# Kernel tuning notes

Measured on AMD Instinct MI355X. Metric: run time of the kernel, lower is better.

## Reference

```python
import jax, jax.numpy as jnp
from jax import lax
import numpy as np

SHAPE = (64, 64, 64)  # spatial grid (D, H, W)
N_PTS = 100000        # active voxels
KPAD = (1, 2, 2)      # 'same' padding for (3,5,5) kernel


def _conv(x, w, pad):
    # x: [B,D,H,W,C], w: [kd,kh,kw,Cin,Cout]
    return lax.conv_general_dilated(
        x, w, window_strides=(1, 1, 1),
        padding=[(p, p) for p in pad],
        dimension_numbers=('NDHWC', 'DHWIO', 'NDHWC'))


def _sparse_maxpool2(x, mask):
    # spconv SparseMaxPool3d(2,2): output active where any input in 2x2x2
    # window is active; value = max over active inputs only.
    neg = jnp.float32(-1e30)
    xm = jnp.where(mask > 0, x, neg)
    win = (1, 2, 2, 2, 1)
    y = lax.reduce_window(xm, neg, lax.max, win, win, 'VALID')
    m2 = lax.reduce_window(mask, jnp.float32(0), lax.max, win, win, 'VALID')
    return jnp.where(m2 > 0, y, 0.0), m2


def setup_inputs() -> dict:
    rng = np.random.default_rng(0)
    D, H, W = SHAPE
    lin = rng.choice(D * H * W, size=N_PTS, replace=False)  # unique voxels
    z = lin // (H * W)
    y = (lin // W) % H
    x = lin % W
    coors = np.stack([np.zeros(N_PTS, np.int32), z, y, x], 1).astype(np.int32)

    key = jax.random.key(0)
    ks = jax.random.split(key, 16)
    feats = jax.random.normal(ks[0], (N_PTS, 3), jnp.float32)

    dims = [(3, 64), (64, 64), (64, 96), (96, 96), (96, 128), (128, 128),
            (128, 160), (160, 160), (160, 192), (192, 192), (192, 224),
            (224, 224), (224, 256), (256, 256)]
    inp = {'features': feats, 'coors': jnp.asarray(coors), 'batch_size': 1}
    for i, (ci, co) in enumerate(dims):
        scale = 1.0 / np.sqrt(ci * 75.0)  # 75 = 3*5*5 kernel taps
        inp[f'w{i}'] = jax.random.normal(ks[i + 1], (3, 5, 5, ci, co),
                                         jnp.float32) * scale
    return inp


def reference(features, coors, batch_size,
              w0, w1, w2, w3, w4, w5, w6, w7, w8, w9, w10, w11, w12, w13):
    # Densify the sparse tensor: inactive voxels are exactly zero, so a dense
    # conv followed by masking to the active set reproduces submanifold conv.
    b, z, y, x = coors[:, 0], coors[:, 1], coors[:, 2], coors[:, 3]
    dense = jnp.zeros((1,) + SHAPE + (3,), jnp.float32).at[b, z, y, x].set(features)
    mask = jnp.zeros((1,) + SHAPE + (1,), jnp.float32).at[b, z, y, x].set(1.0)

    ws = [w0, w1, w2, w3, w4, w5, w6, w7, w8, w9, w10, w11]
    h = dense
    wi = 0
    for _lvl in range(6):  # 6 (subm, subm, pool2) stages
        h = _conv(h, ws[wi], KPAD) * mask; wi += 1
        h = _conv(h, ws[wi], KPAD) * mask; wi += 1
        h, mask = _sparse_maxpool2(h, mask)

    # SparseConv3d(224,256,(3,5,5),padding=(1,2,2)): output active set is the
    # dilation of the input active set by the kernel footprint.
    m2 = lax.reduce_window(mask, jnp.float32(0), lax.max,
                           (1, 3, 5, 5, 1), (1, 1, 1, 1, 1),
                           [(0, 0), (1, 1), (2, 2), (2, 2), (0, 0)])
    h = _conv(h, w12, KPAD) * m2
    mask = m2
    # final SubMConv3d(256,256)
    h = _conv(h, w13, KPAD) * mask
    return h  # [1,1,1,1,256]
```

## Files before the change

kernel.cpp:

```cpp
#include <hip/hip_runtime.h>
#include <hip/hip_bf16.h>
#include <cstdint>

typedef __attribute__((ext_vector_type(8))) short bf16x8;
typedef __attribute__((ext_vector_type(4))) float f32x4;

__device__ __forceinline__ unsigned short f2bf_hi(float v) {
    unsigned u = __float_as_uint(v);
    u = u + 0x7fffu + ((u >> 16) & 1u);
    return (unsigned short)(u >> 16);
}
__device__ __forceinline__ float bf2f(unsigned short h) {
    return __uint_as_float(((unsigned)h) << 16);
}

__global__ void scatter_kernel(const float* __restrict__ feats,
                               const int* __restrict__ coors,
                               float* __restrict__ dense,
                               float* __restrict__ mask, int n)
{
    int i = blockIdx.x * blockDim.x + threadIdx.x;
    if (i >= n) return;
    const int z = coors[i * 4 + 1];
    const int y = coors[i * 4 + 2];
    const int x = coors[i * 4 + 3];
    const size_t s = (size_t)((z * 64 + y) * 64 + x);
    dense[s * 3 + 0] = feats[i * 3 + 0];
    dense[s * 3 + 1] = feats[i * 3 + 1];
    dense[s * 3 + 2] = feats[i * 3 + 2];
    mask[s] = 1.f;
}

__global__ void wprep_kernel(const float* __restrict__ w,
                             unsigned short* __restrict__ wv, int CI, int CO)
{
    const int total = 75 * CI * CO;
    const int stride = gridDim.x * blockDim.x;
    for (int i = blockIdx.x * blockDim.x + threadIdx.x; i < total; i += stride) {
        const int tap = i / (CI * CO);
        const int r = i - tap * CI * CO;
        const int ci = r / CO;
        const int co = r - ci * CO;
        const size_t o = ((size_t)(tap * (CI / 8) + (ci >> 3)) * CO + co) * 8 + (ci & 7);
        wv[o] = f2bf_hi(w[i]);
    }
}

__global__ void wprep2_kernel(const float* __restrict__ w,
                              unsigned short* __restrict__ wv, int CI, int CO)
{
    const int total = 75 * CI * CO;
    const int stride = gridDim.x * blockDim.x;
    for (int i = blockIdx.x * blockDim.x + threadIdx.x; i < total; i += stride) {
        const int tap = i / (CI * CO);
        const int r = i - tap * CI * CO;
        const int ci = r / CO;
        const int co = r - ci * CO;
        const float v = w[i];
        const unsigned short h = f2bf_hi(v);
        const unsigned short l = f2bf_hi(v - bf2f(h));
        const size_t o = ((size_t)(tap * (CI / 8) + (ci >> 3)) * CO + co) * 16 + (ci & 7);
        wv[o] = h; wv[o + 8] = l;
    }
}

__global__ __launch_bounds__(256)
void conv1_kernel(const float* __restrict__ in, const float* __restrict__ w,
                  const float* __restrict__ mask, unsigned short* __restrict__ ob)
{
    constexpr int S = 64, SP = 68;
    __shared__ float lds[15][3][SP];

    const int bid = blockIdx.y * S + blockIdx.x;
    const int wg = (bid & 7) * (S * S / 8) + (bid >> 3);
    const int y = wg & 63, z = wg >> 6;
    const int t = threadIdx.x;

    for (int idx = t; idx < 15 * 3 * SP; idx += 256) {
        const int r = idx / (3 * SP);
        const int rem = idx - r * 3 * SP;
        const int ci = rem / SP;
        const int x = rem - ci * SP;
        const int kz = r / 5, ky = r - kz * 5;
        const int zz = z + kz - 1, yy = y + ky - 2, xi = x - 2;
        float v = 0.f;
        if ((unsigned)zz < (unsigned)S && (unsigned)yy < (unsigned)S && (unsigned)xi < (unsigned)S)
            v = in[(size_t)((zz * S + yy) * S + xi) * 3 + ci];
        lds[r][ci][x] = v;
    }
    __syncthreads();

    const int co = t & 63, xs = t >> 6;
    float acc[16];
#pragma unroll
    for (int i = 0; i < 16; ++i) acc[i] = 0.f;

#pragma unroll 1
    for (int r = 0; r < 15; ++r) {
#pragma unroll
        for (int ci = 0; ci < 3; ++ci) {
            float inv[20];
#pragma unroll
            for (int j = 0; j < 5; ++j)
                *(float4*)&inv[j * 4] = *(const float4*)&lds[r][ci][xs * 16 + j * 4];
            const float* wp = w + (size_t)(r * 15 + ci) * 64 + co;
#pragma unroll
            for (int kx = 0; kx < 5; ++kx) {
                const float wv = wp[kx * 192];
#pragma unroll
                for (int i = 0; i < 16; ++i) acc[i] += inv[i + kx] * wv;
            }
        }
    }

    const size_t vb = (size_t)(z * S + y) * S;
#pragma unroll
    for (int i = 0; i < 16; ++i) {
        const int x = xs * 16 + i;
        const float keep = (mask[vb + x] > 0.f) ? 1.f : 0.f;
        ob[(vb + x) * 64 + co] = f2bf_hi(acc[i] * keep);
    }
}

template<int CIN, int COUT, int S, int YB, int YG, int WN, int NG, int OMODE>
__global__ __launch_bounds__(YG * NG * 64)
void mfma_conv7(const unsigned short* __restrict__ ab,
                const unsigned short* __restrict__ wv,
                const float* __restrict__ mask, float* __restrict__ outf,
                unsigned short* __restrict__ outb)
{
    constexpr int SP = S + 4;
    constexpr int MX = S / 16;
    constexpr int KC = CIN / 32;
    constexpr int KC4 = CIN / 8;
    constexpr int RS = (KC4 <= 8) ? 8 : 16;
    constexpr int PLANE = SP * RS;
    constexpr int NLR = SP * KC4;
    constexpr int NL = 2 * NLR;
    constexpr int NW = YG * NG;
    constexpr int NT = NW * 64;
    constexpr int SREG = (NL + NT - 1) / NT;
    constexpr int YBW = YB / YG;
    constexpr int NYB = S / YB;
    constexpr int JP = (YB + 4) / 2;
    constexpr int NP = 3 * JP;
    static_assert(COUT / 16 == WN * NG, "geometry");
    static_assert((YB + 4) % 2 == 0, "YB even");

    __shared__ unsigned short lds[2 * 2 * PLANE * 8];

    const int bid = blockIdx.y * NYB + blockIdx.x;
    constexpr int NWG = NYB * S;
    const int wg = (bid & 7) * (NWG / 8) + (bid >> 3);
    const int yb = wg % NYB, z = wg / NYB;
    const int y0 = yb * YB;

    const int t = threadIdx.x;
    const int lane = t & 63;
    const int wave = t >> 6;
    const int waveN = wave % NG;
    const int waveY = wave / NG;
    const int col = lane & 15;
    const int ci8 = lane >> 4;

    f32x4 acc[YBW][MX][WN];
    const f32x4 vzero = {0.f, 0.f, 0.f, 0.f};
#pragma unroll
    for (int q = 0; q < YBW; ++q)
#pragma unroll
        for (int m = 0; m < MX; ++m)
#pragma unroll
            for (int n = 0; n < WN; ++n) acc[q][m][n] = vzero;

    uint4 reg[SREG];

    auto issue = [&](int ph) {
        const int kz = ph / JP, jp = ph - kz * JP;
        const int zz = z + kz - 1;
        const bool zv = ((unsigned)zz < (unsigned)S);
#pragma unroll
        for (int i = 0; i < SREG; ++i) {
            const int L = i * NT + t;
            uint4 v = {0u, 0u, 0u, 0u};
            if (L < NL) {
                const int jr = L / NLR;
                const int l2 = L - jr * NLR;
                const int x = l2 / KC4;
                const int c3 = l2 - x * KC4;
                const int xi = x - 2;
                const int yy = y0 + jp * 2 + jr - 2;
                if (zv && (unsigned)yy < (unsigned)S && (unsigned)xi < (unsigned)S)
                    v = *(const uint4*)(ab + (size_t)((zz * S + yy) * S + xi) * CIN + c3 * 8);
            }
            reg[i] = v;
        }
    };
    auto store = [&](int pl) {
#pragma unroll
        for (int i = 0; i < SREG; ++i) {
            const int L = i * NT + t;
            if (L < NL) {
                const int jr = L / NLR;
                const int l2 = L - jr * NLR;
                const int x = l2 / KC4;
                const int c3 = l2 - x * KC4;
                const int p = x * RS + (c3 ^ (x & 7));
                *(uint4*)&lds[((pl * 2 + jr) * PLANE + p) * 8] = reg[i];
            }
        }
    };

    issue(0);
    store(0);
    if (NP > 1) issue(1);
    __syncthreads();

    int cur = 0;
#pragma unroll 1
    for (int ph = 0; ph < NP; ++ph) {
        const int kz = ph / JP, jp = ph - kz * JP;
        const int zz = z + kz - 1;
        if ((unsigned)zz < (unsigned)S) {
#pragma unroll
            for (int jr = 0; jr < 2; ++jr) {
                const int j = jp * 2 + jr;
                const int yy = y0 + j - 2;
                if ((unsigned)yy >= (unsigned)S) continue;
                const unsigned short* plane = lds + (cur * 2 + jr) * PLANE * 8;

                bool vq[YBW];
                int tapb[YBW];
#pragma unroll
                for (int ql = 0; ql < YBW; ++ql) {
                    const int q = waveY * YBW + ql;
                    const int ky = j - q;
                    vq[ql] = (ky >= 0 && ky <= 4);
                    tapb[ql] = (kz * 5 + (vq[ql] ? ky : 0)) * 5;
                }

                bf16x8 wA[YBW][KC][WN], wB[YBW][KC][WN];
                auto wload = [&](bf16x8 (&wb)[YBW][KC][WN], int kx) {
#pragma unroll
                    for (int ql = 0; ql < YBW; ++ql) if (vq[ql]) {
                        const int tap = tapb[ql] + kx;
#pragma unroll
                        for (int kc = 0; kc < KC; ++kc) {
                            const int c3 = kc * 4 + ci8;
#pragma unroll
                            for (int n = 0; n < WN; ++n) {
                                const int co = (waveN * WN + n) * 16 + col;
                                wb[ql][kc][n] = *(const bf16x8*)(wv + ((size_t)(tap * KC4 + c3) * COUT + co) * 8);
                            }
                        }
                    }
                };
                auto wmfma = [&](bf16x8 (&wb)[YBW][KC][WN], bf16x8 (&a)[KC][MX]) {
#pragma unroll
                    for (int ql = 0; ql < YBW; ++ql) if (vq[ql])
#pragma unroll
                        for (int kc = 0; kc < KC; ++kc)
#pragma unroll
                            for (int m = 0; m < MX; ++m)
#pragma unroll
                                for (int n = 0; n < WN; ++n)
                                    acc[ql][m][n] = __builtin_amdgcn_mfma_f32_16x16x32_bf16(a[kc][m], wb[ql][kc][n], acc[ql][m][n], 0, 0, 0);
                };

                wload(wA, 0);
                __builtin_amdgcn_s_setprio(1);
#pragma unroll
                for (int kx = 0; kx < 5; ++kx) {
                    bf16x8 a[KC][MX];
#pragma unroll
                    for (int kc = 0; kc < KC; ++kc) {
                        const int c3 = kc * 4 + ci8;
#pragma unroll
                        for (int m = 0; m < MX; ++m) {
                            const int x = m * 16 + col + kx;
                            const int p = x * RS + (c3 ^ (x & 7));
                            a[kc][m] = *(const bf16x8*)&plane[p * 8];
                        }
                    }
                    if ((kx & 1) == 0) {
                        if (kx + 1 < 5) wload(wB, kx + 1);
                        wmfma(wA, a);
                    } else {
                        if (kx + 1 < 5) wload(wA, kx + 1);
                        wmfma(wB, a);
                    }
                }
                __builtin_amdgcn_s_setprio(0);
            }
        }
        if (ph + 1 < NP) store(cur ^ 1);
        if (ph + 2 < NP) issue(ph + 2);
        __syncthreads();
        cur ^= 1;
    }

    const int rq = lane >> 4;
#pragma unroll
    for (int ql = 0; ql < YBW; ++ql) {
        const int y = y0 + waveY * YBW + ql;
        const size_t vb = (size_t)(z * S + y) * S;
#pragma unroll
        for (int m = 0; m < MX; ++m) {
            const int xb = m * 16 + rq * 4;
#pragma unroll
            for (int r = 0; r < 4; ++r) {
                const int x = xb + r;
                const float keep = (mask[vb + x] > 0.f) ? 1.f : 0.f;
#pragma unroll
                for (int n = 0; n < WN; ++n) {
                    const int co = (waveN * WN + n) * 16 + col;
                    const float v = acc[ql][m][n][r] * keep;
                    if (OMODE == 0) outf[(vb + x) * COUT + co] = v;
                    else            outb[(vb + x) * COUT + co] = f2bf_hi(v);
                }
            }
        }
    }
}

template<int CIN, int COUT, int S, int YB, int YG, int WN, int NG, int OMODE>
__global__ __launch_bounds__(YG * NG * 64)
void mfma_conv6(const unsigned short* __restrict__ ab,
                const unsigned short* __restrict__ wv,
                const float* __restrict__ mask, float* __restrict__ outf,
                unsigned short* __restrict__ outb)
{
    constexpr int SP = S + 4;
    constexpr int MX = S / 16;
    constexpr int KC = CIN / 32;
    constexpr int KC4 = CIN / 8;
    constexpr int RS = (KC4 <= 8) ? 8 : 16;
    constexpr int PLANE = SP * RS;
    constexpr int NL = SP * KC4;
    constexpr int NW = YG * NG;
    constexpr int NT = NW * 64;
    constexpr int SREG = (NL + NT - 1) / NT;
    constexpr int YBW = YB / YG;
    constexpr int NYB = S / YB;
    constexpr int NP = 3 * (YB + 4);
    static_assert(COUT / 16 == WN * NG, "geometry");

    __shared__ unsigned short lds[2 * PLANE * 8];

    const int bid = blockIdx.y * NYB + blockIdx.x;
    constexpr int NWG = NYB * S;
    const int wg = (bid & 7) * (NWG / 8) + (bid >> 3);
    const int yb = wg % NYB, z = wg / NYB;
    const int y0 = yb * YB;

    const int t = threadIdx.x;
    const int lane = t & 63;
    const int wave = t >> 6;
    const int waveN = wave % NG;
    const int waveY = wave / NG;
    const int col = lane & 15;
    const int ci8 = lane >> 4;

    f32x4 acc[YBW][MX][WN];
    const f32x4 vzero = {0.f, 0.f, 0.f, 0.f};
#pragma unroll
    for (int q = 0; q < YBW; ++q)
#pragma unroll
        for (int m = 0; m < MX; ++m)
#pragma unroll
            for (int n = 0; n < WN; ++n) acc[q][m][n] = vzero;

    uint4 reg[SREG];

    auto issue = [&](int ph) {
        const int kz = ph / (YB + 4), j = ph - kz * (YB + 4);
        const int zz = z + kz - 1, yy = y0 + j - 2;
        const bool rv = ((unsigned)zz < (unsigned)S) && ((unsigned)yy < (unsigned)S);
        const size_t rowbase = rv ? (size_t)((zz * S + yy) * S) * CIN : 0;
#pragma unroll
        for (int i = 0; i < SREG; ++i) {
            const int L = i * NT + t;
            uint4 v = {0u, 0u, 0u, 0u};
            if (L < NL) {
                const int x = L / KC4;
                const int c3 = L - x * KC4;
                const int xi = x - 2;
                if (rv && (unsigned)xi < (unsigned)S)
                    v = *(const uint4*)(ab + rowbase + (size_t)xi * CIN + c3 * 8);
            }
            reg[i] = v;
        }
    };
    auto store = [&](int pl) {
#pragma unroll
        for (int i = 0; i < SREG; ++i) {
            const int L = i * NT + t;
            if (L < NL) {
                const int x = L / KC4;
                const int c3 = L - x * KC4;
                const int p = x * RS + (c3 ^ (x & 7));
                *(uint4*)&lds[(pl * PLANE + p) * 8] = reg[i];
            }
        }
    };

    issue(0);
    store(0);
    if (NP > 1) issue(1);
    __syncthreads();

    int cur = 0;
#pragma unroll 1
    for (int ph = 0; ph < NP; ++ph) {
        const int kz = ph / (YB + 4), j = ph - kz * (YB + 4);
        const int zz = z + kz - 1, yy = y0 + j - 2;
        if (((unsigned)zz < (unsigned)S) && ((unsigned)yy < (unsigned)S)) {
            const unsigned short* plane = lds + cur * PLANE * 8;

            bool vq[YBW];
            int tapb[YBW];
#pragma unroll
            for (int ql = 0; ql < YBW; ++ql) {
                const int q = waveY * YBW + ql;
                const int ky = j - q;
                vq[ql] = (ky >= 0 && ky <= 4);
                tapb[ql] = (kz * 5 + (vq[ql] ? ky : 0)) * 5;
            }

            bf16x8 wA[YBW][KC][WN], wB[YBW][KC][WN];
            auto wload = [&](bf16x8 (&wb)[YBW][KC][WN], int kx) {
#pragma unroll
                for (int ql = 0; ql < YBW; ++ql) if (vq[ql]) {
                    const int tap = tapb[ql] + kx;
#pragma unroll
                    for (int kc = 0; kc < KC; ++kc) {
                        const int c3 = kc * 4 + ci8;
#pragma unroll
                        for (int n = 0; n < WN; ++n) {
                            const int co = (waveN * WN + n) * 16 + col;
                            wb[ql][kc][n] = *(const bf16x8*)(wv + ((size_t)(tap * KC4 + c3) * COUT + co) * 8);
                        }
                    }
                }
            };
            auto wmfma = [&](bf16x8 (&wb)[YBW][KC][WN], bf16x8 (&a)[KC][MX]) {
#pragma unroll
                for (int ql = 0; ql < YBW; ++ql) if (vq[ql])
#pragma unroll
                    for (int kc = 0; kc < KC; ++kc)
#pragma unroll
                        for (int m = 0; m < MX; ++m)
#pragma unroll
                            for (int n = 0; n < WN; ++n)
                                acc[ql][m][n] = __builtin_amdgcn_mfma_f32_16x16x32_bf16(a[kc][m], wb[ql][kc][n], acc[ql][m][n], 0, 0, 0);
            };

            wload(wA, 0);
            __builtin_amdgcn_s_setprio(1);
#pragma unroll
            for (int kx = 0; kx < 5; ++kx) {
                bf16x8 a[KC][MX];
#pragma unroll
                for (int kc = 0; kc < KC; ++kc) {
                    const int c3 = kc * 4 + ci8;
#pragma unroll
                    for (int m = 0; m < MX; ++m) {
                        const int x = m * 16 + col + kx;
                        const int p = x * RS + (c3 ^ (x & 7));
                        a[kc][m] = *(const bf16x8*)&plane[p * 8];
                    }
                }
                if ((kx & 1) == 0) {
                    if (kx + 1 < 5) wload(wB, kx + 1);
                    wmfma(wA, a);
                } else {
                    if (kx + 1 < 5) wload(wA, kx + 1);
                    wmfma(wB, a);
                }
            }
            __builtin_amdgcn_s_setprio(0);
        }
        if (ph + 1 < NP) store(cur ^ 1);
        if (ph + 2 < NP) issue(ph + 2);
        __syncthreads();
        cur ^= 1;
    }

    const int rq = lane >> 4;
#pragma unroll
    for (int ql = 0; ql < YBW; ++ql) {
        const int y = y0 + waveY * YBW + ql;
        const size_t vb = (size_t)(z * S + y) * S;
#pragma unroll
        for (int m = 0; m < MX; ++m) {
            const int xb = m * 16 + rq * 4;
#pragma unroll
            for (int r = 0; r < 4; ++r) {
                const int x = xb + r;
                const float keep = (mask[vb + x] > 0.f) ? 1.f : 0.f;
#pragma unroll
                for (int n = 0; n < WN; ++n) {
                    const int co = (waveN * WN + n) * 16 + col;
                    const float v = acc[ql][m][n][r] * keep;
                    if (OMODE == 0) outf[(vb + x) * COUT + co] = v;
                    else            outb[(vb + x) * COUT + co] = f2bf_hi(v);
                }
            }
        }
    }
}

template<int CIN, int COUT, int S, int NW>
__global__ __launch_bounds__(NW * 64)
void dgemm2_kernel(const unsigned short* __restrict__ inb,
                   const unsigned short* __restrict__ wv,
                   const float* __restrict__ mask,
                   unsigned short* __restrict__ outb)
{
    constexpr int M = S * S * S;
    constexpr int KC = CIN / 32;
    constexpr int KC4 = CIN / 8;
    __shared__ f32x4 part[NW][64];

    const int t = threadIdx.x;
    const int lane = t & 63;
    const int w = t >> 6;
    const int col = lane & 15;
    const int g = lane >> 4;

    const int va = blockIdx.x * 16 + col;
    const bool av = (va < M);
    const int az = (va / (S * S)) % S;
    const int ay = (va / S) % S;
    const int ax = va % S;
    const int co = blockIdx.y * 16 + col;

    f32x4 acc0 = {0.f, 0.f, 0.f, 0.f};
    f32x4 acc1 = {0.f, 0.f, 0.f, 0.f};

#pragma unroll 2
    for (int tap = w; tap < 75; tap += NW) {
        const int dz = tap / 25 - 1;
        const int dy = (tap / 5) % 5 - 2;
        const int dx = tap % 5 - 2;
        const int zz = az + dz, yy = ay + dy, xx = ax + dx;
        const bool valid = av && ((unsigned)zz < (unsigned)S) &&
                           ((unsigned)yy < (unsigned)S) && ((unsigned)xx < (unsigned)S);
        const size_t abase = valid ? (size_t)((zz * S + yy) * S + xx) * CIN : 0;
#pragma unroll
        for (int kc = 0; kc < KC; ++kc) {
            const int c3 = kc * 4 + g;
            bf16x8 a = {0, 0, 0, 0, 0, 0, 0, 0};
            if (valid) a = *(const bf16x8*)(inb + abase + c3 * 8);
            const unsigned short* wp = wv + ((size_t)(tap * KC4 + c3) * COUT + co) * 16;
            bf16x8 wh = *(const bf16x8*)wp;
            bf16x8 wl = *(const bf16x8*)(wp + 8);
            acc0 = __builtin_amdgcn_mfma_f32_16x16x32_bf16(a, wh, acc0, 0, 0, 0);
            acc1 = __builtin_amdgcn_mfma_f32_16x16x32_bf16(a, wl, acc1, 0, 0, 0);
        }
    }

    part[w][lane] = acc0 + acc1;
    __syncthreads();

    if (w == 0) {
        f32x4 s = part[0][lane];
#pragma unroll
        for (int i = 1; i < NW; ++i) s += part[i][lane];
#pragma unroll
        for (int r = 0; r < 4; ++r) {
            const int v = blockIdx.x * 16 + g * 4 + r;
            if (v < M) {
                const float keep = (mask[v] > 0.f) ? 1.f : 0.f;
                outb[(size_t)v * COUT + co] = f2bf_hi(s[r] * keep);
            }
        }
    }
}

__global__ void pool_bf8_kernel(const unsigned short* __restrict__ inb,
                                const float* __restrict__ mi,
                                unsigned short* __restrict__ outb,
                                float* __restrict__ mo, int S, int C)
{
    const int So = S >> 1;
    const int C8 = C >> 3;
    const long long total = (long long)So * So * So * C8;
    for (long long i = blockIdx.x * (long long)blockDim.x + threadIdx.x; i < total;
         i += (long long)gridDim.x * blockDim.x) {
        const int c8 = (int)(i % C8);
        const long long s = i / C8;
        const int xo = (int)(s % So);
        const int yo = (int)((s / So) % So);
        const int zo = (int)(s / ((long long)So * So));
        float best[8];
#pragma unroll
        for (int k = 0; k < 8; ++k) best[k] = -1e30f;
        float m2 = 0.f;
        for (int dz = 0; dz < 2; ++dz)
            for (int dy = 0; dy < 2; ++dy)
                for (int dx = 0; dx < 2; ++dx) {
                    const int zi = zo * 2 + dz, yi = yo * 2 + dy, xi = xo * 2 + dx;
                    const float m = mi[(zi * S + yi) * S + xi];
                    if (m > 0.f) {
                        m2 = 1.f;
                        const unsigned short* p =
                            inb + ((size_t)((zi * S + yi) * S + xi) * C8 + c8) * 8;
                        uint4 v = *(const uint4*)p;
                        const unsigned short* vs = (const unsigned short*)&v;
#pragma unroll
                        for (int k = 0; k < 8; ++k) best[k] = fmaxf(best[k], bf2f(vs[k]));
                    }
                }
        uint4 o;
        unsigned short* os = (unsigned short*)&o;
#pragma unroll
        for (int k = 0; k < 8; ++k) os[k] = f2bf_hi((m2 > 0.f) ? best[k] : 0.f);
        *(uint4*)(outb + i * 8) = o;
        if (c8 == 0) mo[s] = m2;
    }
}

__global__ __launch_bounds__(256)
void final_kernel(const unsigned short* __restrict__ h, const float* __restrict__ mask,
                  const float* __restrict__ w12, const float* __restrict__ w13,
                  float* __restrict__ out)
{
    __shared__ float o1[256];
    const int co = threadIdx.x;
    const float m = (mask[0] > 0.f) ? 1.f : 0.f;
    float a = 0.f;
    for (int ci = 0; ci < 224; ++ci)
        a += bf2f(h[ci]) * w12[(size_t)(37 * 224 + ci) * 256 + co];
    o1[co] = a * m;
    __syncthreads();
    float b = 0.f;
    for (int ci = 0; ci < 256; ++ci)
        b += o1[ci] * w13[(size_t)(37 * 256 + ci) * 256 + co];
    out[co] = b * m;
}

static void pool_bf8(const unsigned short* inb, const float* mi,
                     unsigned short* outb, float* mo, int S, int C, hipStream_t stream)
{
    const long long total = (long long)(S / 2) * (S / 2) * (S / 2) * (C / 8);
    long long grid = (total + 255) / 256;
    if (grid > 4096) grid = 4096;
    if (grid < 1) grid = 1;
    pool_bf8_kernel<<<(int)grid, 256, 0, stream>>>(inb, mi, outb, mo, S, C);
}

#define WOFF0 0
#define WOFF1 307200
#define WOFF2 768000
#define WOFF3 1459200
#define WOFF4 2380800
#define DOFF6 0
#define DOFF7 3072000
#define DOFF8 6912000
#define DOFF9 11520000
#define DOFF10 17049600
#define DOFF11 23500800

extern "C" void kernel_launch(void* const* d_in, const int* in_sizes, int n_in,
                              void* d_out, int out_size, void* d_ws, size_t ws_size,
                              hipStream_t stream)
{
    const float* feats = (const float*)d_in[0];
    const int*   coors = (const int*)d_in[1];
    const float* w[14];
    for (int i = 0; i < 14; ++i) w[i] = (const float*)d_in[3 + i];
    float* outp = (float*)d_out;

    float* dense0 = (float*)d_ws;
    float* mA = dense0 + 786432;
    float* mB = mA + 262144;
    unsigned short* ab = (unsigned short*)(mB + 262144);
    unsigned short* bb = ab + 16777216;
    unsigned short* wvp = bb + 16777216;
    unsigned short* wdp = wvp + 3609600;

    const int npts = in_sizes[0] / 3;

    wprep_kernel<<<256, 256, 0, stream>>>(w[1], wvp + WOFF0, 64, 64);
    wprep_kernel<<<256, 256, 0, stream>>>(w[2], wvp + WOFF1, 64, 96);
    wprep_kernel<<<256, 256, 0, stream>>>(w[3], wvp + WOFF2, 96, 96);
    wprep_kernel<<<256, 256, 0, stream>>>(w[4], wvp + WOFF3, 96, 128);
    wprep_kernel<<<256, 256, 0, stream>>>(w[5], wvp + WOFF4, 128, 128);
    wprep2_kernel<<<256, 256, 0, stream>>>(w[6], wdp + DOFF6, 128, 160);
    wprep2_kernel<<<256, 256, 0, stream>>>(w[7], wdp + DOFF7, 160, 160);
    wprep2_kernel<<<256, 256, 0, stream>>>(w[8], wdp + DOFF8, 160, 192);
    wprep2_kernel<<<256, 256, 0, stream>>>(w[9], wdp + DOFF9, 192, 192);
    wprep2_kernel<<<256, 256, 0, stream>>>(w[10], wdp + DOFF10, 192, 224);
    wprep2_kernel<<<256, 256, 0, stream>>>(w[11], wdp + DOFF11, 224, 224);

    hipMemsetAsync(dense0, 0, (size_t)786432 * sizeof(float), stream);
    hipMemsetAsync(mA, 0, (size_t)262144 * sizeof(float), stream);
    scatter_kernel<<<(npts + 255) / 256, 256, 0, stream>>>(feats, coors, dense0, mA, npts);

    conv1_kernel<<<dim3(64, 64), 256, 0, stream>>>(dense0, w[0], mA, ab);
    mfma_conv7<64, 64, 64, 4, 2, 2, 2, 1><<<dim3(16, 64), 256, 0, stream>>>(
        ab, wvp + WOFF0, mA, nullptr, bb);
    pool_bf8(bb, mA, ab, mB, 64, 64, stream);
    mfma_conv6<64, 96, 32, 2, 1, 2, 3, 1><<<dim3(16, 32), 192, 0, stream>>>(
        ab, wvp + WOFF1, mB, nullptr, bb);
    mfma_conv6<96, 96, 32, 2, 1, 2, 3, 1><<<dim3(16, 32), 192, 0, stream>>>(
        bb, wvp + WOFF2, mB, nullptr, ab);
    pool_bf8(ab, mB, bb, mA, 32, 96, stream);
    mfma_conv7<96, 128, 16, 2, 1, 2, 4, 1><<<dim3(8, 16), 256, 0, stream>>>(
        bb, wvp + WOFF3, mA, nullptr, ab);
    mfma_conv7<128, 128, 16, 2, 1, 2, 4, 1><<<dim3(8, 16), 256, 0, stream>>>(
        ab, wvp + WOFF4, mA, nullptr, bb);
    pool_bf8(bb, mA, ab, mB, 16, 128, stream);
    dgemm2_kernel<128, 160, 8, 4><<<dim3(32, 10), 256, 0, stream>>>(ab, wdp + DOFF6, mB, bb);
    dgemm2_kernel<160, 160, 8, 4><<<dim3(32, 10), 256, 0, stream>>>(bb, wdp + DOFF7, mB, ab);
    pool_bf8(ab, mB, bb, mA, 8, 160, stream);
    dgemm2_kernel<160, 192, 4, 8><<<dim3(4, 12), 512, 0, stream>>>(bb, wdp + DOFF8, mA, ab);
    dgemm2_kernel<192, 192, 4, 8><<<dim3(4, 12), 512, 0, stream>>>(ab, wdp + DOFF9, mA, bb);
    pool_bf8(bb, mA, ab, mB, 4, 192, stream);
    dgemm2_kernel<192, 224, 2, 8><<<dim3(1, 14), 512, 0, stream>>>(ab, wdp + DOFF10, mB, bb);
    dgemm2_kernel<224, 224, 2, 8><<<dim3(1, 14), 512, 0, stream>>>(bb, wdp + DOFF11, mB, ab);
    pool_bf8(ab, mB, bb, mA, 2, 224, stream);
    final_kernel<<<1, 256, 0, stream>>>(bb, mA, w[12], w[13], outp);
}
```

Baseline: 871.9 us.

## Add single-row MFMA conv kernel for 16^3 level and widen weight prep grids

Adds a new MFMA conv kernel that gives each block one (z,y) output row. It double-buffers the 15 kz/ky input planes in swizzled LDS and ping-pongs weight registers across kx taps. The kernel is used for the two 16^3 convolutions, doubling the block count from 128 to 256 so more CUs stay busy on this small level. The weight-prep launches also grow from 256 to 2048 blocks to parallelise that setup. The trade-off is that each block does less work, so plane loads and weight traffic are repeated more often per output.

Result: faster. 783.2 us (-10.2%).

```diff
diff --git a/kernel.cpp b/kernel.cpp
--- a/kernel.cpp
+++ b/kernel.cpp
@@ -509,6 +509,165 @@
     }
 }
 
+template<int CIN, int COUT, int S, int WM, int WN, int MG, int NG, int OMODE>
+__global__ __launch_bounds__(MG * NG * 64)
+void mfma_conv3c(const unsigned short* __restrict__ ab,
+                 const unsigned short* __restrict__ wv,
+                 const float* __restrict__ mask, float* __restrict__ outf,
+                 unsigned short* __restrict__ outb)
+{
+    constexpr int SP = S + 4;
+    constexpr int KC = CIN / 32;
+    constexpr int KC4 = CIN / 8;
+    constexpr int RS = (KC4 <= 8) ? 8 : 16;
+    constexpr int PLANE = SP * RS;
+    constexpr int NL = SP * KC4;
+    constexpr int NT = MG * NG * 64;
+    constexpr int SREG = (NL + NT - 1) / NT;
+    static_assert(S / 16 == WM * MG && COUT / 16 == WN * NG, "geometry");
+
+    __shared__ unsigned short lds[2 * PLANE * 8];
+
+    const int bid = blockIdx.y * S + blockIdx.x;
+    const int wg = (bid & 7) * (S * S / 8) + (bid >> 3);
+    const int y = wg % S, z = wg / S;
+
+    const int t = threadIdx.x;
+    const int lane = t & 63;
+    const int wave = t >> 6;
+    const int waveM = wave % MG;
+    const int waveN = wave / MG;
+    const int col = lane & 15;
+    const int ci8 = lane >> 4;
+
+    f32x4 acc[WM][WN];
+    const f32x4 vzero = {0.f, 0.f, 0.f, 0.f};
+#pragma unroll
+    for (int m = 0; m < WM; ++m)
+#pragma unroll
+        for (int n = 0; n < WN; ++n) acc[m][n] = vzero;
+
+    uint4 reg[SREG];
+
+    auto issue = [&](int kzy) {
+        const int kz = kzy / 5, ky = kzy - kz * 5;
+        const int zz = z + kz - 1, yy = y + ky - 2;
+        const bool rv = ((unsigned)zz < (unsigned)S) && ((unsigned)yy < (unsigned)S);
+        const size_t rowbase = rv ? (size_t)((zz * S + yy) * S) * CIN : 0;
+#pragma unroll
+        for (int i = 0; i < SREG; ++i) {
+            const int L = i * NT + t;
+            uint4 v = {0u, 0u, 0u, 0u};
+            if (L < NL) {
+                const int x = L / KC4;
+                const int c3 = L - x * KC4;
+                const int xi = x - 2;
+                if (rv && (unsigned)xi < (unsigned)S)
+                    v = *(const uint4*)(ab + rowbase + (size_t)xi * CIN + c3 * 8);
+            }
+            reg[i] = v;
+        }
+    };
+    auto store = [&](int pl) {
+#pragma unroll
+        for (int i = 0; i < SREG; ++i) {
+            const int L = i * NT + t;
+            if (L < NL) {
+                const int x = L / KC4;
+                const int c3 = L - x * KC4;
+                const int p = x * RS + (c3 ^ (x & 7));
+                *(uint4*)&lds[(pl * PLANE + p) * 8] = reg[i];
+            }
+        }
+    };
+
+    issue(0);
+    store(0);
+    issue(1);
+    __syncthreads();
+
+    int cur = 0;
+#pragma unroll 1
+    for (int kzy = 0; kzy < 15; ++kzy) {
+        const int kz = kzy / 5, ky = kzy - kz * 5;
+        const int zz = z + kz - 1, yy = y + ky - 2;
+        if (((unsigned)zz < (unsigned)S) && ((unsigned)yy < (unsigned)S)) {
+            const unsigned short* plane = lds + cur * PLANE * 8;
+
+            bf16x8 wA[KC][WN], wB[KC][WN];
+            auto wload = [&](bf16x8 (&wb)[KC][WN], int kx) {
+                const int tap = kzy * 5 + kx;
+#pragma unroll
+                for (int kc = 0; kc < KC; ++kc) {
+                    const int c3 = kc * 4 + ci8;
+#pragma unroll
+                    for (int n = 0; n < WN; ++n) {
+                        const int co = (waveN * WN + n) * 16 + col;
+                        wb[kc][n] = *(const bf16x8*)(wv + ((size_t)(tap * KC4 + c3) * COUT + co) * 8);
+                    }
+                }
+            };
+            auto wmfma = [&](bf16x8 (&wb)[KC][WN], bf16x8 (&a)[KC][WM]) {
+#pragma unroll
+                for (int kc = 0; kc < KC; ++kc)
+#pragma unroll
+                    for (int m = 0; m < WM; ++m)
+#pragma unroll
+                        for (int n = 0; n < WN; ++n)
+                            acc[m][n] = __builtin_amdgcn_mfma_f32_16x16x32_bf16(a[kc][m], wb[kc][n], acc[m][n], 0, 0, 0);
+            };
+
+            wload(wA, 0);
+            __builtin_amdgcn_s_setprio(1);
+#pragma unroll
+            for (int kx = 0; kx < 5; ++kx) {
+                bf16x8 a[KC][WM];
+#pragma unroll
+                for (int kc = 0; kc < KC; ++kc) {
+                    const int c3 = kc * 4 + ci8;
+#pragma unroll
+                    for (int m = 0; m < WM; ++m) {
+                        const int x = (waveM * WM + m) * 16 + col + kx;
+                        const int p = x * RS + (c3 ^ (x & 7));
+                        a[kc][m] = *(const bf16x8*)&plane[p * 8];
+                    }
+                }
+                if ((kx & 1) == 0) {
+                    if (kx + 1 < 5) wload(wB, kx + 1);
+                    wmfma(wA, a);
+                } else {
+                    if (kx + 1 < 5) wload(wA, kx + 1);
+                    wmfma(wB, a);
+                }
+            }
+            __builtin_amdgcn_s_setprio(0);
+        }
+        if (kzy + 1 < 15) store(cur ^ 1);
+        if (kzy + 2 < 15) issue(kzy + 2);
+        __syncthreads();
+        cur ^= 1;
+    }
+
+    const int rq = lane >> 4;
+    const size_t vb = (size_t)(z * S + y) * S;
+#pragma unroll
+    for (int m = 0; m < WM; ++m) {
+        const int xb = (waveM * WM + m) * 16 + rq * 4;
+#pragma unroll
+        for (int r = 0; r < 4; ++r) {
+            const int x = xb + r;
+            const float keep = (mask[vb + x] > 0.f) ? 1.f : 0.f;
+#pragma unroll
+            for (int n = 0; n < WN; ++n) {
+                const int co = (waveN * WN + n) * 16 + col;
+                const float v = acc[m][n][r] * keep;
+                if (OMODE == 0) outf[(vb + x) * COUT + co] = v;
+                else            outb[(vb + x) * COUT + co] = f2bf_hi(v);
+            }
+        }
+    }
+}
+
 template<int CIN, int COUT, int S, int NW>
 __global__ __launch_bounds__(NW * 64)
 void dgemm2_kernel(const unsigned short* __restrict__ inb,
@@ -681,17 +840,17 @@
 
     const int npts = in_sizes[0] / 3;
 
-    wprep_kernel<<<256, 256, 0, stream>>>(w[1], wvp + WOFF0, 64, 64);
-    wprep_kernel<<<256, 256, 0, stream>>>(w[2], wvp + WOFF1, 64, 96);
-    wprep_kernel<<<256, 256, 0, stream>>>(w[3], wvp + WOFF2, 96, 96);
-    wprep_kernel<<<256, 256, 0, stream>>>(w[4], wvp + WOFF3, 96, 128);
-    wprep_kernel<<<256, 256, 0, stream>>>(w[5], wvp + WOFF4, 128, 128);
-    wprep2_kernel<<<256, 256, 0, stream>>>(w[6], wdp + DOFF6, 128, 160);
-    wprep2_kernel<<<256, 256, 0, stream>>>(w[7], wdp + DOFF7, 160, 160);
-    wprep2_kernel<<<256, 256, 0, stream>>>(w[8], wdp + DOFF8, 160, 192);
-    wprep2_kernel<<<256, 256, 0, stream>>>(w[9], wdp + DOFF9, 192, 192);
-    wprep2_kernel<<<256, 256, 0, stream>>>(w[10], wdp + DOFF10, 192, 224);
-    wprep2_kernel<<<256, 256, 0, stream>>>(w[11], wdp + DOFF11, 224, 224);
+    wprep_kernel<<<2048, 256, 0, stream>>>(w[1], wvp + WOFF0, 64, 64);
+    wprep_kernel<<<2048, 256, 0, stream>>>(w[2], wvp + WOFF1, 64, 96);
+    wprep_kernel<<<2048, 256, 0, stream>>>(w[3], wvp + WOFF2, 96, 96);
+    wprep_kernel<<<2048, 256, 0, stream>>>(w[4], wvp + WOFF3, 96, 128);
+    wprep_kernel<<<2048, 256, 0, stream>>>(w[5], wvp + WOFF4, 128, 128);
+    wprep2_kernel<<<2048, 256, 0, stream>>>(w[6], wdp + DOFF6, 128, 160);
+    wprep2_kernel<<<2048, 256, 0, stream>>>(w[7], wdp + DOFF7, 160, 160);
+    wprep2_kernel<<<2048, 256, 0, stream>>>(w[8], wdp + DOFF8, 160, 192);
+    wprep2_kernel<<<2048, 256, 0, stream>>>(w[9], wdp + DOFF9, 192, 192);
+    wprep2_kernel<<<2048, 256, 0, stream>>>(w[10], wdp + DOFF10, 192, 224);
+    wprep2_kernel<<<2048, 256, 0, stream>>>(w[11], wdp + DOFF11, 224, 224);
 
     hipMemsetAsync(dense0, 0, (size_t)786432 * sizeof(float), stream);
     hipMemsetAsync(mA, 0, (size_t)262144 * sizeof(float), stream);
@@ -706,9 +865,9 @@
     mfma_conv6<96, 96, 32, 2, 1, 2, 3, 1><<<dim3(16, 32), 192, 0, stream>>>(
         bb, wvp + WOFF2, mB, nullptr, ab);
     pool_bf8(ab, mB, bb, mA, 32, 96, stream);
-    mfma_conv7<96, 128, 16, 2, 1, 2, 4, 1><<<dim3(8, 16), 256, 0, stream>>>(
+    mfma_conv3c<96, 128, 16, 1, 2, 1, 4, 1><<<dim3(16, 16), 256, 0, stream>>>(
         bb, wvp + WOFF3, mA, nullptr, ab);
-    mfma_conv7<128, 128, 16, 2, 1, 2, 4, 1><<<dim3(8, 16), 256, 0, stream>>>(
+    mfma_conv3c<128, 128, 16, 1, 2, 1, 4, 1><<<dim3(16, 16), 256, 0, stream>>>(
         ab, wvp + WOFF4, mA, nullptr, bb);
     pool_bf8(bb, mA, ab, mB, 16, 128, stream);
     dgemm2_kernel<128, 160, 8, 4><<<dim3(32, 10), 256, 0, stream>>>(ab, wdp + DOFF6, mB, bb);
```
